# Optimization experiments

Measured on AMD Instinct MI355X. Metric: run time of the kernel, lower is better.

## Reference

```python
import jax, jax.numpy as jnp
import numpy as np

EMBED_DIM = 384

def setup_inputs() -> dict:
    key = jax.random.key(0)
    k1, k2, k3 = jax.random.split(key, 3)
    B, P, N, d = 8, 4, 4096, EMBED_DIM
    hidden_states = jax.random.normal(k1, (B, P, N, d), dtype=jnp.float32)
    # 1x1 conv == pointwise linear over channel dim; scale like fan-in init
    w_qkv = jax.random.normal(k2, (d, 1 + 2 * d), dtype=jnp.float32) * (1.0 / np.sqrt(d))
    b_qkv = jnp.zeros((1 + 2 * d,), dtype=jnp.float32)
    w_out = jax.random.normal(k3, (d, d), dtype=jnp.float32) * (1.0 / np.sqrt(d))
    b_out = jnp.zeros((d,), dtype=jnp.float32)
    return {"hidden_states": hidden_states, "w_qkv": w_qkv, "b_qkv": b_qkv,
            "w_out": w_out, "b_out": b_out}

def reference(hidden_states, w_qkv, b_qkv, w_out, b_out):
    d = EMBED_DIM
    # qkv 1x1 conv (channels-last): [B,P,N,d] @ [d, 1+2d]
    qkv = jnp.einsum("bpnd,de->bpne", hidden_states, w_qkv) + b_qkv
    query = qkv[..., :1]                # [B,P,N,1]
    key_ = qkv[..., 1:1 + d]            # [B,P,N,d]
    value = qkv[..., 1 + d:]            # [B,P,N,d]
    # softmax over token axis (axis=2); attn_dropout=0.0 -> identity
    context_scores = jax.nn.softmax(query, axis=2)
    # softmax-weighted pooling of keys over tokens -> [B,P,1,d]
    context_vector = jnp.sum(key_ * context_scores, axis=2, keepdims=True)
    # relu-gated broadcast multiply
    out = context_vector * jax.nn.relu(value)
    # out 1x1 conv
    out = jnp.einsum("bpnd,de->bpne", out, w_out) + b_out
    return out
```

## Files before the change

kernel.cpp:

```cpp
#include <hip/hip_runtime.h>

#define D     384
#define E     769
#define NTOK  4096
#define BPN   32
#define NCH   64

typedef short s16x8 __attribute__((ext_vector_type(8)));
typedef float f32x4 __attribute__((ext_vector_type(4)));
typedef float f32x2 __attribute__((ext_vector_type(2)));

__device__ __forceinline__ unsigned short f2bf(float f){
  unsigned int u = __builtin_bit_cast(unsigned int, f);
  u += 0x7FFFu + ((u >> 16) & 1u);
  return (unsigned short)(u >> 16);
}

__global__ void k0_prep(const float* __restrict__ wqkv, const float* __restrict__ wout,
                        float* __restrict__ wq, unsigned short* __restrict__ wvF,
                        unsigned short* __restrict__ woF){
  int tid = blockIdx.x*256 + threadIdx.x;
  if (tid < D) wq[tid] = wqkv[(size_t)tid*E];
  if (tid < 24*12*64*8){
    int pos = tid & 7;
    int lane = (tid >> 3) & 63;
    int kt  = (tid >> 9) % 12;
    int nt  = tid / 6144;
    int l15 = lane & 15, l4 = lane >> 4;
    int col = nt*16 + l15;
    int k   = kt*32 + l4*8 + pos;
    wvF[tid] = f2bf(wqkv[(size_t)k*E + 385 + col]);
    woF[tid] = f2bf(wout[(size_t)k*D + col]);
  }
}

__global__ __launch_bounds__(384)
void kA_fused(const float* __restrict__ H, const float* __restrict__ wq,
              float* __restrict__ partial, float* __restrict__ mArr,
              float* __restrict__ lArr){
  __shared__ float Hs[32][D];
  __shared__ float qs[32];
  __shared__ float ws[32];
  __shared__ float scaleS;
  const int ch = blockIdx.x, bp = blockIdx.y;
  const int t = threadIdx.x;
  const int wave = t >> 6, lane = t & 63;

  f32x2 wqr[3];
  #pragma unroll
  for (int seg=0;seg<3;++seg)
    wqr[seg] = *reinterpret_cast<const f32x2*>(wq + lane*2 + seg*128);

  const size_t base0 = (size_t)bp*NTOK + (size_t)ch*64;

  f32x2 h[6][3];
  #pragma unroll
  for (int j=0;j<6;++j){
    int r = wave + j*6;
    if (r < 32){
      const float* hr = H + (base0 + r)*D + lane*2;
      #pragma unroll
      for (int seg=0;seg<3;++seg)
        h[j][seg] = *reinterpret_cast<const f32x2*>(hr + seg*128);
    }
  }
  #pragma unroll
  for (int j=0;j<6;++j){
    int r = wave + j*6;
    if (r < 32){
      float a = 0.f;
      #pragma unroll
      for (int seg=0;seg<3;++seg){
        *reinterpret_cast<f32x2*>(&Hs[r][lane*2 + seg*128]) = h[j][seg];
        a += h[j][seg].x*wqr[seg].x + h[j][seg].y*wqr[seg].y;
      }
      #pragma unroll
      for (int off=32; off; off>>=1) a += __shfl_xor(a, off, 64);
      if (lane == 0) qs[r] = a;
    }
  }
  __syncthreads();

  float acc = 0.f;
  float mRun = -3.4e38f, lRun = 0.f;

  #pragma unroll 1
  for (int s=0; s<2; ++s){
    if (s == 0){
      #pragma unroll
      for (int j=0;j<6;++j){
        int r = wave + j*6;
        if (r < 32){
          const float* hr = H + (base0 + 32 + r)*D + lane*2;
          #pragma unroll
          for (int seg=0;seg<3;++seg)
            h[j][seg] = *reinterpret_cast<const f32x2*>(hr + seg*128);
        }
      }
    }

    if (wave == 0){
      float q = (lane < 32) ? qs[lane] : -3.4e38f;
      float msub = q;
      #pragma unroll
      for (int off=32; off; off>>=1) msub = fmaxf(msub, __shfl_xor(msub, off, 64));
      float mNew = fmaxf(mRun, msub);
      float sc   = __expf(mRun - mNew);
      float e    = (lane < 32) ? __expf(q - mNew) : 0.f;
      if (lane < 32) ws[lane] = e;
      float lsub = e;
      #pragma unroll
      for (int off=32; off; off>>=1) lsub += __shfl_xor(lsub, off, 64);
      lRun = lRun*sc + lsub;
      mRun = mNew;
      if (lane == 0) scaleS = sc;
    }
    __syncthreads();

    float sc = scaleS;
    float a2 = 0.f;
    #pragma unroll 8
    for (int n=0;n<32;++n)
      a2 += ws[n] * Hs[n][t];
    acc = acc*sc + a2;
    __syncthreads();

    if (s == 0){
      #pragma unroll
      for (int j=0;j<6;++j){
        int r = wave + j*6;
        if (r < 32){
          float a = 0.f;
          #pragma unroll
          for (int seg=0;seg<3;++seg){
            *reinterpret_cast<f32x2*>(&Hs[r][lane*2 + seg*128]) = h[j][seg];
            a += h[j][seg].x*wqr[seg].x + h[j][seg].y*wqr[seg].y;
          }
          #pragma unroll
          for (int off=32; off; off>>=1) a += __shfl_xor(a, off, 64);
          if (lane == 0) qs[r] = a;
        }
      }
      __syncthreads();
    }
  }

  partial[((size_t)bp*NCH + ch)*D + t] = acc;
  if (t == 0){ mArr[bp*NCH + ch] = mRun; lArr[bp*NCH + ch] = lRun; }
}

__global__ void kB_cv(const float* __restrict__ partial, const float* __restrict__ mArr,
                      const float* __restrict__ lArr, const float* __restrict__ wqkv,
                      const float* __restrict__ bqkv, float* __restrict__ cv){
  __shared__ float S[D];
  const int bp = blockIdx.x, t = threadIdx.x;
  float M = -3.4e38f;
  #pragma unroll 4
  for (int c = 0; c < NCH; ++c) M = fmaxf(M, mArr[bp*NCH + c]);
  float num = 0.f, den = 0.f;
  #pragma unroll 2
  for (int c = 0; c < NCH; ++c){
    float f = __expf(mArr[bp*NCH + c] - M);
    num += f * partial[((size_t)bp*NCH + c)*D + t];
    den += f * lArr[bp*NCH + c];
  }
  S[t] = num / den;
  __syncthreads();
  float acc = bqkv[1 + t];
  #pragma unroll 4
  for (int k = 0; k < D; ++k)
    acc += S[k] * wqkv[(size_t)k*E + 1 + t];
  cv[(size_t)bp*D + t] = acc;
}

#define BM 64
#define LOADW(W, kt, n) (*reinterpret_cast<const s16x8*>(&(W)[((size_t)((n)*12+(kt))*64 + lane)*8]))

__global__ __launch_bounds__(512, 2)
void k5_main(const float* __restrict__ H, const unsigned short* __restrict__ wvF,
             const unsigned short* __restrict__ woF, const float* __restrict__ cv,
             const float* __restrict__ bqkv, const float* __restrict__ bout,
             float* __restrict__ out){
  __shared__ unsigned short As[BM*D];
  const int bp = blockIdx.y;
  const int m0 = blockIdx.x*BM;
  const size_t rowbase = (size_t)bp*NTOK + m0;
  const float* A = H + rowbase*D;
  const int t = threadIdx.x;
  const int wave = t>>6, lane = t&63;
  const int l15 = lane&15, l4 = lane>>4;
  const int n0 = wave*48;
  const unsigned short* wvW = wvF + (size_t)wave*3*12*512;
  const unsigned short* woW = woF + (size_t)wave*3*12*512;

  #pragma unroll
  for (int i=0;i<12;++i){
    int c = t + i*512;
    int idx8 = c >> 1;
    int l15v = idx8 & 15;
    int l4v  = (idx8 >> 4) & 3;
    int ktv  = (idx8 >> 6) % 12;
    int mv   = idx8 / 768;
    f32x4 v = *reinterpret_cast<const f32x4*>(
        A + (size_t)(mv*16 + l15v)*D + ktv*32 + l4v*8 + (c&1)*4);
    ushort4 b;
    b.x=f2bf(v.x); b.y=f2bf(v.y); b.z=f2bf(v.z); b.w=f2bf(v.w);
    *reinterpret_cast<ushort4*>(&As[c*4]) = b;
  }

  s16x8 b0[3], b1[3];
  #pragma unroll
  for (int n=0;n<3;++n) b0[n] = LOADW(wvW, 0, n);
  #pragma unroll
  for (int n=0;n<3;++n) b1[n] = LOADW(wvW, 1, n);
  __syncthreads();

  f32x4 acc[4][3] = {};
  #pragma unroll
  for (int kt=0; kt<12; ++kt){
    s16x8 bp_[3];
    if (kt < 10){
      #pragma unroll
      for (int n=0;n<3;++n) bp_[n] = LOADW(wvW, kt+2, n);
    }
    s16x8 a[4];
    #pragma unroll
    for (int m=0;m<4;++m)
      a[m] = *reinterpret_cast<const s16x8*>(&As[((m*12+kt)*64 + lane)*8]);
    #pragma unroll
    for (int m=0;m<4;++m)
      #pragma unroll
      for (int n=0;n<3;++n)
        acc[m][n] = __builtin_amdgcn_mfma_f32_16x16x32_bf16(a[m], b0[n], acc[m][n], 0,0,0);
    #pragma unroll
    for (int n=0;n<3;++n){ b0[n] = b1[n]; b1[n] = bp_[n]; }
  }

  float bv[3], cvv[3];
  #pragma unroll
  for (int n=0;n<3;++n){
    int col = n0 + n*16 + l15;
    bv[n]  = bqkv[385+col];
    cvv[n] = cv[(size_t)bp*D + col];
  }
  #pragma unroll
  for (int n=0;n<3;++n) b0[n] = LOADW(woW, 0, n);
  #pragma unroll
  for (int n=0;n<3;++n) b1[n] = LOADW(woW, 1, n);
  __syncthreads();

  #pragma unroll
  for (int n=0;n<3;++n){
    int col  = n0 + n*16 + l15;
    int kt2  = col >> 5;
    int l42  = (col >> 3) & 3;
    int pos2 = col & 7;
    #pragma unroll
    for (int m=0;m<4;++m){
      #pragma unroll
      for (int r=0;r<4;++r){
        int row = l4*4 + r;
        float v = acc[m][n][r] + bv[n];
        v = v > 0.f ? v*cvv[n] : 0.f;
        As[((m*12+kt2)*64 + l42*16 + row)*8 + pos2] = f2bf(v);
      }
    }
  }
  #pragma unroll
  for (int m=0;m<4;++m)
    #pragma unroll
    for (int n=0;n<3;++n)
      acc[m][n] = (f32x4){0.f,0.f,0.f,0.f};
  __syncthreads();

  #pragma unroll
  for (int kt=0; kt<12; ++kt){
    s16x8 bp_[3];
    if (kt < 10){
      #pragma unroll
      for (int n=0;n<3;++n) bp_[n] = LOADW(woW, kt+2, n);
    }
    s16x8 a[4];
    #pragma unroll
    for (int m=0;m<4;++m)
      a[m] = *reinterpret_cast<const s16x8*>(&As[((m*12+kt)*64 + lane)*8]);
    #pragma unroll
    for (int m=0;m<4;++m)
      #pragma unroll
      for (int n=0;n<3;++n)
        acc[m][n] = __builtin_amdgcn_mfma_f32_16x16x32_bf16(a[m], b0[n], acc[m][n], 0,0,0);
    #pragma unroll
    for (int n=0;n<3;++n){ b0[n] = b1[n]; b1[n] = bp_[n]; }
  }

  #pragma unroll
  for (int n=0;n<3;++n){
    int col = n0 + n*16 + l15;
    float bo = bout[col];
    #pragma unroll
    for (int m=0;m<4;++m)
      #pragma unroll
      for (int r=0;r<4;++r){
        int row = m*16 + l4*4 + r;
        out[(rowbase+row)*D + col] = acc[m][n][r] + bo;
      }
  }
}

extern "C" void kernel_launch(void* const* d_in, const int* in_sizes, int n_in,
                              void* d_out, int out_size, void* d_ws, size_t ws_size,
                              hipStream_t stream){
  const float* H    = (const float*)d_in[0];
  const float* wqkv = (const float*)d_in[1];
  const float* bqkv = (const float*)d_in[2];
  const float* wout = (const float*)d_in[3];
  const float* bout = (const float*)d_in[4];
  float* out = (float*)d_out;

  char* ws = (char*)d_ws;
  float*          partial = (float*)(ws + 0x000000);
  float*          mArr    = (float*)(ws + 0x300000);
  float*          lArr    = (float*)(ws + 0x302000);
  float*          cv      = (float*)(ws + 0x304000);
  float*          wq      = (float*)(ws + 0x310000);
  unsigned short* wvF     = (unsigned short*)(ws + 0x311000);
  unsigned short* woF     = (unsigned short*)(ws + 0x359000);

  hipLaunchKernelGGL(k0_prep,  dim3(576),          dim3(256), 0, stream, wqkv, wout, wq, wvF, woF);
  hipLaunchKernelGGL(kA_fused, dim3(NCH, BPN),     dim3(384), 0, stream, H, wq, partial, mArr, lArr);
  hipLaunchKernelGGL(kB_cv,    dim3(BPN),          dim3(384), 0, stream, partial, mArr, lArr, wqkv, bqkv, cv);
  hipLaunchKernelGGL(k5_main,  dim3(NTOK/BM, BPN), dim3(512), 0, stream, H, wvF, woF, cv, bqkv, bout, out);
}
```

Baseline: 224.5 us.

## Restructure softmax-pooling kernel to keep tokens in registers and reduce across waves

The first-pass pooling kernel now runs with 8 waves of 512 threads, each wave owning 4 token rows per 32-token step. The softmax-weighted key sum is computed directly from the row values held in registers, so the full 32x384 shared-memory tile and its transposed re-read are no longer needed. A small cross-wave reduction through shared memory produces the per-chunk partial sum. This removes shared-memory traffic and one barrier per step, but drops the explicit prefetch of the second half of the chunk that overlapped loads with compute.

Result: no change. 221.2 us (median of 2 runs) (-1.5%).

```diff
diff --git a/kernel.cpp b/kernel.cpp
--- a/kernel.cpp
+++ b/kernel.cpp
@@ -34,72 +34,53 @@
   }
 }
 
-__global__ __launch_bounds__(384)
+__global__ __launch_bounds__(512)
 void kA_fused(const float* __restrict__ H, const float* __restrict__ wq,
               float* __restrict__ partial, float* __restrict__ mArr,
               float* __restrict__ lArr){
-  __shared__ float Hs[32][D];
+  __shared__ float red[8][392];
   __shared__ float qs[32];
   __shared__ float ws[32];
   __shared__ float scaleS;
   const int ch = blockIdx.x, bp = blockIdx.y;
-  const int t = threadIdx.x;
-  const int wave = t >> 6, lane = t & 63;
+  const int t = threadIdx.x, w = t >> 6, lane = t & 63;
+  const size_t base0 = (size_t)bp*NTOK + (size_t)ch*64;
 
   f32x2 wqr[3];
   #pragma unroll
   for (int seg=0;seg<3;++seg)
     wqr[seg] = *reinterpret_cast<const f32x2*>(wq + lane*2 + seg*128);
 
-  const size_t base0 = (size_t)bp*NTOK + (size_t)ch*64;
-
-  f32x2 h[6][3];
-  #pragma unroll
-  for (int j=0;j<6;++j){
-    int r = wave + j*6;
-    if (r < 32){
-      const float* hr = H + (base0 + r)*D + lane*2;
+  float acc6[6] = {0.f,0.f,0.f,0.f,0.f,0.f};
+  float mRun = -3.4e38f, lRun = 0.f;
+
+  #pragma unroll 1
+  for (int s=0; s<2; ++s){
+    f32x2 h[4][3];
+    #pragma unroll
+    for (int j=0;j<4;++j){
+      const float* hr = H + (base0 + (size_t)(s*32 + w*4 + j))*D + lane*2;
       #pragma unroll
       for (int seg=0;seg<3;++seg)
         h[j][seg] = *reinterpret_cast<const f32x2*>(hr + seg*128);
     }
-  }
-  #pragma unroll
-  for (int j=0;j<6;++j){
-    int r = wave + j*6;
-    if (r < 32){
-      float a = 0.f;
-      #pragma unroll
-      for (int seg=0;seg<3;++seg){
-        *reinterpret_cast<f32x2*>(&Hs[r][lane*2 + seg*128]) = h[j][seg];
-        a += h[j][seg].x*wqr[seg].x + h[j][seg].y*wqr[seg].y;
-      }
-      #pragma unroll
-      for (int off=32; off; off>>=1) a += __shfl_xor(a, off, 64);
-      if (lane == 0) qs[r] = a;
-    }
-  }
-  __syncthreads();
-
-  float acc = 0.f;
-  float mRun = -3.4e38f, lRun = 0.f;
-
-  #pragma unroll 1
-  for (int s=0; s<2; ++s){
-    if (s == 0){
-      #pragma unroll
-      for (int j=0;j<6;++j){
-        int r = wave + j*6;
-        if (r < 32){
-          const float* hr = H + (base0 + 32 + r)*D + lane*2;
-          #pragma unroll
-          for (int seg=0;seg<3;++seg)
-            h[j][seg] = *reinterpret_cast<const f32x2*>(hr + seg*128);
-        }
-      }
-    }
-
-    if (wave == 0){
+    float a[4];
+    #pragma unroll
+    for (int j=0;j<4;++j)
+      a[j] = h[j][0].x*wqr[0].x + h[j][0].y*wqr[0].y
+           + h[j][1].x*wqr[1].x + h[j][1].y*wqr[1].y
+           + h[j][2].x*wqr[2].x + h[j][2].y*wqr[2].y;
+    #pragma unroll
+    for (int off=32; off; off>>=1){
+      #pragma unroll
+      for (int j=0;j<4;++j) a[j] += __shfl_xor(a[j], off, 64);
+    }
+    if (lane == 0){
+      qs[w*4+0]=a[0]; qs[w*4+1]=a[1]; qs[w*4+2]=a[2]; qs[w*4+3]=a[3];
+    }
+    __syncthreads();
+
+    if (w == 0){
       float q = (lane < 32) ? qs[lane] : -3.4e38f;
       float msub = q;
       #pragma unroll
@@ -117,35 +98,31 @@
     }
     __syncthreads();
 
-    float sc = scaleS;
-    float a2 = 0.f;
-    #pragma unroll 8
-    for (int n=0;n<32;++n)
-      a2 += ws[n] * Hs[n][t];
-    acc = acc*sc + a2;
-    __syncthreads();
-
-    if (s == 0){
-      #pragma unroll
-      for (int j=0;j<6;++j){
-        int r = wave + j*6;
-        if (r < 32){
-          float a = 0.f;
-          #pragma unroll
-          for (int seg=0;seg<3;++seg){
-            *reinterpret_cast<f32x2*>(&Hs[r][lane*2 + seg*128]) = h[j][seg];
-            a += h[j][seg].x*wqr[seg].x + h[j][seg].y*wqr[seg].y;
-          }
-          #pragma unroll
-          for (int off=32; off; off>>=1) a += __shfl_xor(a, off, 64);
-          if (lane == 0) qs[r] = a;
-        }
-      }
-      __syncthreads();
-    }
-  }
-
-  partial[((size_t)bp*NCH + ch)*D + t] = acc;
+    float sc  = scaleS;
+    float wj0 = ws[w*4+0], wj1 = ws[w*4+1], wj2 = ws[w*4+2], wj3 = ws[w*4+3];
+    #pragma unroll
+    for (int seg=0;seg<3;++seg){
+      acc6[seg*2]   = acc6[seg*2]*sc
+                    + wj0*h[0][seg].x + wj1*h[1][seg].x
+                    + wj2*h[2][seg].x + wj3*h[3][seg].x;
+      acc6[seg*2+1] = acc6[seg*2+1]*sc
+                    + wj0*h[0][seg].y + wj1*h[1][seg].y
+                    + wj2*h[2][seg].y + wj3*h[3][seg].y;
+    }
+  }
+
+  #pragma unroll
+  for (int seg=0;seg<3;++seg){
+    red[w][lane*2+seg*128]   = acc6[seg*2];
+    red[w][lane*2+seg*128+1] = acc6[seg*2+1];
+  }
+  __syncthreads();
+  if (t < D){
+    float s8 = 0.f;
+    #pragma unroll
+    for (int w8=0;w8<8;++w8) s8 += red[w8][t];
+    partial[((size_t)bp*NCH + ch)*D + t] = s8;
+  }
   if (t == 0){ mArr[bp*NCH + ch] = mRun; lArr[bp*NCH + ch] = lRun; }
 }
 
@@ -327,7 +304,7 @@
   unsigned short* woF     = (unsigned short*)(ws + 0x359000);
 
   hipLaunchKernelGGL(k0_prep,  dim3(576),          dim3(256), 0, stream, wqkv, wout, wq, wvF, woF);
-  hipLaunchKernelGGL(kA_fused, dim3(NCH, BPN),     dim3(384), 0, stream, H, wq, partial, mArr, lArr);
+  hipLaunchKernelGGL(kA_fused, dim3(NCH, BPN),     dim3(512), 0, stream, H, wq, partial, mArr, lArr);
   hipLaunchKernelGGL(kB_cv,    dim3(BPN),          dim3(384), 0, stream, partial, mArr, lArr, wqkv, bqkv, cv);
   hipLaunchKernelGGL(k5_main,  dim3(NTOK/BM, BPN), dim3(512), 0, stream, H, wvF, woF, cv, bqkv, bout, out);
 }
```
